# Kernel optimization log

Measured on AMD Instinct MI355X. Metric: run time of the kernel, lower is better.

## Reference

```python
import jax, jax.numpy as jnp
from jax import lax
import numpy as np

L = 4          # n_layers
H = 1024       # hidden_units
IN = 128       # input feature dim
OUT = 128      # out_size
B = 64         # batch
T = 512        # seq_len


def setup_inputs() -> dict:
    key = jax.random.key(0)
    ks = jax.random.split(key, 10)
    def glorot(k, shape):
        fan_in, fan_out = shape[-2], shape[-1]
        lim = np.sqrt(6.0 / (fan_in + fan_out)).astype(np.float32)
        return jax.random.uniform(k, shape, jnp.float32, -lim, lim)
    return {
        "x": jax.random.normal(ks[0], (B, T, IN), jnp.float32),
        "Wi": glorot(ks[1], (IN, H)),          # i_proj kernel
        "bi": jnp.zeros((H,), jnp.float32),     # i_proj bias
        "Wh": glorot(ks[2], (L, 2 * H, H)),     # per-layer Dense(Wh) kernel on concat([x,h])
        "bh_dense": jnp.zeros((L, H), jnp.float32),  # Dense(Wh) bias
        "bh": jnp.zeros((L, H), jnp.float32),        # extra bh weight
        "Wy": glorot(ks[3], (L, H, H)),         # per-layer Dense(Wy) kernel
        "by_dense": jnp.zeros((L, H), jnp.float32),  # Dense(Wy) bias
        "by": jnp.zeros((L, H), jnp.float32),        # extra by weight
        "Wo": glorot(ks[4], (H, OUT)),          # o_proj kernel
        "bo_dense": jnp.zeros((OUT,), jnp.float32),  # o_proj bias
        "o_bias": jnp.zeros((OUT,), jnp.float32),    # extra o_bias weight
    }


def reference(x, Wi, bi, Wh, bh_dense, bh, Wy, by_dense, by, Wo, bo_dense, o_bias):
    # decode() path, dropout as identity (deterministic reference).
    x_proj = x @ Wi + bi                      # [B, T, H]
    xs = jnp.transpose(x_proj, (1, 0, 2))     # time-major [T, B, H]
    h0 = jnp.zeros((L, B, H), x.dtype)

    def step(h_prev, xt):                     # h_prev [L,B,H], xt [B,H]
        inp = xt
        h_new = []
        for m in range(L):
            xc = jnp.concatenate([inp, h_prev[m]], axis=1)          # [B, 2H]
            h = jax.nn.relu(xc @ Wh[m] + bh_dense[m] + bh[m])       # [B, H]
            y = h @ Wy[m] + by_dense[m] + by[m]                     # [B, H]
            out = y + inp          # RNNLayer residual
            out = out + inp        # RNNNetwork residual (applied twice, faithful)
            h_new.append(h)
            inp = out
        return jnp.stack(h_new, axis=0), inp

    _, dec_states = lax.scan(step, h0, xs)    # dec_states [T, B, H]
    dec_states = jnp.transpose(dec_states, (1, 0, 2))  # [B, T, H]
    return dec_states @ Wo + bo_dense + o_bias         # [B, T, OUT]
```

## Files before the change

### kernel.cpp

```cpp
#include <hip/hip_runtime.h>
#include <cstdint>
#include <cstddef>

namespace {
constexpr int HD  = 1024;
constexpr int LD  = 4;
constexpr int BD  = 64;
constexpr int TD  = 512;
constexpr int IND = 128;
constexpr int OD  = 128;
constexpr int NSLOT = 5;
constexpr int LBH = LD * BD * HD;
constexpr int BH  = BD * HD;
constexpr int UNITS = 2816;
constexpr size_t HH = (size_t)HD * HD;
}

typedef unsigned short ushort_t;
typedef __attribute__((ext_vector_type(8))) short short8x;
typedef __attribute__((ext_vector_type(4))) float f32x4;

__device__ __forceinline__ ushort_t f2bf(float f) {
  unsigned u = __builtin_bit_cast(unsigned, f);
  u += 0x7FFFu + ((u >> 16) & 1u);
  return (ushort_t)(u >> 16);
}
__device__ __forceinline__ float bf2f(ushort_t h) {
  return __builtin_bit_cast(float, (unsigned)h << 16);
}
__device__ __forceinline__ void split3(float f, ushort_t& h1, ushort_t& h2, ushort_t& h3) {
  h1 = f2bf(f); float r = f - bf2f(h1);
  h2 = f2bf(r); r -= bf2f(h2);
  h3 = f2bf(r);
}

__device__ __forceinline__ void gemm_tile(
    const float* __restrict__ A, int lda, const float* __restrict__ Bm, int ldb,
    float* __restrict__ C, int ldc, int K, int row0, int col0,
    float alpha, const float* __restrict__ addvec)
{
  __shared__ float a_lds[64][65];
  __shared__ __align__(16) float b_lds[64][132];
  const int tid = threadIdx.x;
  const int rg = tid >> 4, cg = tid & 15;

  float acc[4][8];
  #pragma unroll
  for (int i = 0; i < 4; ++i)
    #pragma unroll
    for (int j = 0; j < 8; ++j) acc[i][j] = 0.f;

  for (int k0 = 0; k0 < K; k0 += 64) {
    #pragma unroll
    for (int i = 0; i < 4; ++i) {
      const int q = tid + i * 256;
      const int r = q >> 4;
      const int k4 = (q & 15) << 2;
      const float4 v = *(const float4*)(A + (size_t)(row0 + r) * lda + k0 + k4);
      a_lds[r][k4 + 0] = v.x; a_lds[r][k4 + 1] = v.y;
      a_lds[r][k4 + 2] = v.z; a_lds[r][k4 + 3] = v.w;
    }
    #pragma unroll
    for (int i = 0; i < 8; ++i) {
      const int q = tid + i * 256;
      const int k = q >> 5;
      const int c4 = (q & 31) << 2;
      *(float4*)&b_lds[k][c4] = *(const float4*)(Bm + (size_t)(k0 + k) * ldb + col0 + c4);
    }
    __syncthreads();
    #pragma unroll 4
    for (int k = 0; k < 64; ++k) {
      float wv[8], av[4];
      *(float4*)&wv[0] = *(const float4*)&b_lds[k][cg * 8];
      *(float4*)&wv[4] = *(const float4*)&b_lds[k][cg * 8 + 4];
      #pragma unroll
      for (int i = 0; i < 4; ++i) av[i] = a_lds[rg * 4 + i][k];
      #pragma unroll
      for (int i = 0; i < 4; ++i)
        #pragma unroll
        for (int j = 0; j < 8; ++j)
          acc[i][j] = fmaf(av[i], wv[j], acc[i][j]);
    }
    __syncthreads();
  }

  #pragma unroll
  for (int i = 0; i < 4; ++i) {
    const int r = row0 + rg * 4 + i;
    #pragma unroll
    for (int j = 0; j < 8; ++j) {
      const int c = col0 + cg * 8 + j;
      float v = alpha * acc[i][j];
      if (addvec) v += addvec[c];
      C[(size_t)r * ldc + c] = v;
    }
  }
}

__global__ __launch_bounds__(256) void prep1_k(
    const float* __restrict__ Wy, const float* __restrict__ Wh,
    const float* __restrict__ Wi, const float* __restrict__ Wo,
    float* __restrict__ G, float* __restrict__ WiA,
    float* __restrict__ P, float* __restrict__ WiWo)
{
  static const int pj[6] = {0, 0, 1, 0, 1, 2};
  static const int pm[6] = {1, 2, 2, 3, 3, 3};
  const int bid = blockIdx.x;
  const float *A, *Bm; float* C; int lda, ldb, ldc, row0, col0;
  if (bid < 768) {
    const int p = bid >> 7, rr = bid & 127;
    A = Wy + (size_t)pj[p] * HH; lda = HD;
    Bm = Wh + (size_t)pm[p] * 2 * HH; ldb = HD;
    C = G + (size_t)p * HH; ldc = HD;
    row0 = (rr >> 3) * 64; col0 = (rr & 7) * 128;
  } else if (bid < 832) {
    const int r = bid - 768, m = r >> 4;
    A = Wi; lda = HD;
    Bm = Wh + (size_t)m * 2 * HH; ldb = HD;
    C = WiA + (size_t)m * IND * HD; ldc = HD;
    row0 = ((r >> 3) & 1) * 64; col0 = (r & 7) * 128;
  } else if (bid < 896) {
    const int r = bid - 832, j = r >> 4;
    A = Wy + (size_t)j * HH; lda = HD;
    Bm = Wo; ldb = OD;
    C = P + (size_t)j * HD * OD; ldc = OD;
    row0 = (r & 15) * 64; col0 = 0;
  } else {
    const int r = bid - 896;
    A = Wi; lda = HD; Bm = Wo; ldb = OD; C = WiWo; ldc = OD;
    row0 = r * 64; col0 = 0;
  }
  gemm_tile(A, lda, Bm, ldb, C, ldc, HD, row0, col0, 1.f, nullptr);
}

__global__ __launch_bounds__(256) void prep2_k(
    const float* __restrict__ x, const float* __restrict__ WiWo,
    const float* __restrict__ const_o, float* __restrict__ out)
{
  gemm_tile(x, IND, WiWo, OD, out, OD, IND, blockIdx.x * 64, 0, 16.f, const_o);
}

__global__ __launch_bounds__(256) void consts_k(
    const float* __restrict__ Wh, const float* __restrict__ bh_dense, const float* __restrict__ bh,
    const float* __restrict__ by_dense, const float* __restrict__ by, const float* __restrict__ bi,
    const float* __restrict__ Wo, const float* __restrict__ bo_dense, const float* __restrict__ o_bias,
    float* __restrict__ cvec, float* __restrict__ const_o)
{
  __shared__ float e_lds[HD];
  const int tid = threadIdx.x;
  if (blockIdx.x < 16) {
    const int m = blockIdx.x >> 2;
    const int hcol = ((blockIdx.x & 3) << 8) + tid;
    for (int k = tid; k < HD; k += 256) {
      float e = (float)(1 << m) * bi[k];
      for (int j = 0; j < m; ++j)
        e += (float)(1 << (m - 1 - j)) * (by_dense[j * HD + k] + by[j * HD + k]);
      e_lds[k] = e;
    }
    __syncthreads();
    float acc = bh_dense[m * HD + hcol] + bh[m * HD + hcol];
    for (int k = 0; k < HD; ++k)
      acc = fmaf(e_lds[k], Wh[(size_t)m * 2 * HH + (size_t)k * HD + hcol], acc);
    cvec[m * HD + hcol] = acc;
  } else {
    if (tid < OD) {
      float acc = bo_dense[tid] + o_bias[tid];
      for (int k = 0; k < HD; ++k) {
        float e = 16.f * bi[k];
        e += 8.f * (by_dense[0 * HD + k] + by[0 * HD + k]);
        e += 4.f * (by_dense[1 * HD + k] + by[1 * HD + k]);
        e += 2.f * (by_dense[2 * HD + k] + by[2 * HD + k]);
        e += 1.f * (by_dense[3 * HD + k] + by[3 * HD + k]);
        acc = fmaf(e, Wo[(size_t)k * OD + tid], acc);
      }
      const_o[tid] = acc;
    }
  }
}

__global__ __launch_bounds__(256) void prep3_k(
    const float* __restrict__ G, const float* __restrict__ Wh,
    const float* __restrict__ WiA, const float* __restrict__ P,
    ushort_t* __restrict__ wTh, ushort_t* __restrict__ wTx, ushort_t* __restrict__ wTp)
{
  __shared__ ushort_t tl[3][64][66];
  const int tid = threadIdx.x, bid = blockIdx.x;
  const float* src; ushort_t* dstb; int ld, dstK, k0, n0; size_t PS;
  if (bid < 2560) {
    const int mat = bid >> 8, rr = bid & 255;
    k0 = (rr >> 4) * 64; n0 = (rr & 15) * 64;
    src = (mat < 6) ? (G + (size_t)mat * HH) : (Wh + (size_t)(mat - 6) * 2 * HH + HH);
    ld = 1024; dstb = wTh + (size_t)mat * 3 * HH; PS = HH; dstK = 1024;
  } else if (bid < 2688) {
    const int r = bid - 2560, mat = r >> 5, rr = r & 31;
    k0 = (rr >> 4) * 64; n0 = (rr & 15) * 64;
    src = WiA + (size_t)mat * IND * HD; ld = 1024;
    dstb = wTx + (size_t)mat * 3 * 131072; PS = 131072; dstK = 128;
  } else {
    const int r = bid - 2688, mat = r >> 5, rr = r & 31;
    k0 = (rr >> 1) * 64; n0 = (rr & 1) * 64;
    src = P + (size_t)mat * HD * OD; ld = 128;
    dstb = wTp + (size_t)mat * 3 * 131072; PS = 131072; dstK = 1024;
  }
  #pragma unroll
  for (int i = 0; i < 4; ++i) {
    const int q = tid + i * 256, kr = q >> 4, n4 = (q & 15) * 4;
    const float4 vv = *(const float4*)(src + (size_t)(k0 + kr) * ld + n0 + n4);
    ushort_t h1, h2, h3;
    split3(vv.x, h1, h2, h3); tl[0][n4+0][kr]=h1; tl[1][n4+0][kr]=h2; tl[2][n4+0][kr]=h3;
    split3(vv.y, h1, h2, h3); tl[0][n4+1][kr]=h1; tl[1][n4+1][kr]=h2; tl[2][n4+1][kr]=h3;
    split3(vv.z, h1, h2, h3); tl[0][n4+2][kr]=h1; tl[1][n4+2][kr]=h2; tl[2][n4+2][kr]=h3;
    split3(vv.w, h1, h2, h3); tl[0][n4+3][kr]=h1; tl[1][n4+3][kr]=h2; tl[2][n4+3][kr]=h3;
  }
  __syncthreads();
  #pragma unroll
  for (int i = 0; i < 4; ++i) {
    const int q = tid + i * 256, nr = q >> 4, k4 = (q & 15) * 4;
    #pragma unroll
    for (int p = 0; p < 3; ++p) {
      const unsigned lo = (unsigned)tl[p][nr][k4]     | ((unsigned)tl[p][nr][k4+1] << 16);
      const unsigned hi = (unsigned)tl[p][nr][k4 + 2] | ((unsigned)tl[p][nr][k4+3] << 16);
      *(uint2*)(dstb + (size_t)p * PS + (size_t)(n0 + nr) * dstK + k0 + k4) = make_uint2(lo, hi);
    }
  }
}

__global__ __launch_bounds__(256, 3) void rnn_scan_k(
    const float* __restrict__ x,
    const ushort_t* __restrict__ wTh,
    const ushort_t* __restrict__ wTx,
    const ushort_t* __restrict__ wTp,
    const float* __restrict__ cvec,
    float* __restrict__ zring,
    float* __restrict__ outp,
    int* __restrict__ bar, int nblk)
{
  __shared__ __align__(16) ushort_t s_a[3 * 64 * 64];
  __shared__ __align__(16) ushort_t s_b[3 * 64 * 64];
  const int tid = threadIdx.x, bid = blockIdx.x;
  const int lane = tid & 63, wid = tid >> 6;
  const int qr = wid >> 1, qc = wid & 1;
  const int l15 = lane & 15, l4 = lane >> 4;
  const int arow0 = tid & 63, akq = tid >> 6;
  const int bcol = tid >> 2, bks = tid & 3;
  const int u0 = (UNITS * bid) / nblk;
  const int u1 = (UNITS * (bid + 1)) / nblk;
  const int gb[4] = {0, 0, 1, 3};

  const int ar0 = qr * 32 + l15, ar1 = ar0 + 16;
  const int bc0 = qc * 32 + l15, bc1 = bc0 + 16;
  const int oa0b = ar0 * 64, oa1b = ar1 * 64, ob0b = bc0 * 64, ob1b = bc1 * 64;
  const int as0 = ar0 & 7, as1 = ar1 & 7, bs0 = bc0 & 7, bs1 = bc1 & 7;

  int* root = bar + 1024;
  int* gen  = bar + 1056;

  for (int v = 0; v < TD + LD; ++v) {
    {
      float* zp = zring + (size_t)((v + 1) % NSLOT) * LBH;
      for (int i = bid * 256 + tid; i < LBH; i += nblk * 256)
        __hip_atomic_store(&zp[i], 0.f, __ATOMIC_RELAXED, __HIP_MEMORY_SCOPE_AGENT);
    }

    f32x4 c00 = {0.f,0.f,0.f,0.f}, c01 = c00, c10 = c00, c11 = c00;
    float* cur = nullptr;
    int cldd = 0;

    auto flush = [&]() {
      const int colb = qc * 32 + l15;
      const int rowb = qr * 32 + l4 * 4;
      #pragma unroll
      for (int r = 0; r < 4; ++r) {
        atomicAdd(cur + (size_t)(rowb + r) * cldd + colb,           c00[r]);
        atomicAdd(cur + (size_t)(rowb + r) * cldd + colb + 16,      c01[r]);
        atomicAdd(cur + (size_t)(rowb + 16 + r) * cldd + colb,      c10[r]);
        atomicAdd(cur + (size_t)(rowb + 16 + r) * cldd + colb + 16, c11[r]);
      }
      c00 = f32x4{0.f,0.f,0.f,0.f}; c01 = c00; c10 = c00; c11 = c00;
    };

    for (int u = u0; u < u1; ++u) {
      const float* Ab = nullptr; const float* cvp = nullptr;
      const ushort_t* Wt = nullptr;
      float* dst = nullptr;
      int Ars = 0, WK = 0, dstrs = 0; size_t WPS = 0;
      float scale = 1.f;

      if (u < 2688) {
        int m, rel;
        if (u < 288)       { m = 0; rel = u; }
        else if (u < 832)  { m = 1; rel = u - 288; }
        else if (u < 1632) { m = 2; rel = u - 832; }
        else               { m = 3; rel = u - 1632; }
        const int per = (m + 1) * 16 + 2;
        const int cb = rel / per, r2 = rel - cb * per;
        const int t = v - m;
        if (t >= 0 && t < TD) {
          if (r2 < (m + 1) * 16) {
            const int src = r2 >> 4, kc = r2 & 15;
            if (src < m) {
              const int j = src;
              Ab  = zring + (size_t)((t + j) % NSLOT) * LBH + (size_t)j * BH + kc * 64;
              cvp = cvec + j * HD + kc * 64;
              scale = (float)(1 << (m - 1 - j));
              Wt = wTh + (size_t)(gb[m] + j) * 3 * HH + (size_t)(cb * 64) * 1024 + kc * 64;
              Ars = HD; WPS = HH; WK = 1024;
              dst = zring + (size_t)(v % NSLOT) * LBH + (size_t)m * BH + cb * 64;
              dstrs = HD;
            } else if (t >= 1) {
              Ab  = zring + (size_t)((v - 1) % NSLOT) * LBH + (size_t)m * BH + kc * 64;
              cvp = cvec + m * HD + kc * 64;
              scale = 1.f;
              Wt = wTh + (size_t)(6 + m) * 3 * HH + (size_t)(cb * 64) * 1024 + kc * 64;
              Ars = HD; WPS = HH; WK = 1024;
              dst = zring + (size_t)(v % NSLOT) * LBH + (size_t)m * BH + cb * 64;
              dstrs = HD;
            }
          } else {
            const int xk = r2 - (m + 1) * 16;
            Ab = x + (size_t)t * IND + xk * 64;
            Ars = TD * IND; cvp = nullptr;
            scale = (float)(1 << m);
            Wt = wTx + (size_t)m * 3 * 131072 + (size_t)(cb * 64) * 128 + xk * 64;
            WPS = 131072; WK = 128;
            dst = zring + (size_t)(v % NSLOT) * LBH + (size_t)m * BH + cb * 64;
            dstrs = HD;
          }
        }
      } else {
        const int r = u - 2688, j = r >> 5, rr = r & 31, ct = rr >> 4, kc = rr & 15;
        const int tp = v - 1 - j;
        if (tp >= 0 && tp < TD) {
          Ab  = zring + (size_t)((v - 1) % NSLOT) * LBH + (size_t)j * BH + kc * 64;
          Ars = HD;
          cvp = cvec + j * HD + kc * 64;
          scale = (float)(1 << (3 - j));
          Wt = wTp + (size_t)j * 3 * 131072 + (size_t)(ct * 64) * 1024 + kc * 64;
          WPS = 131072; WK = 1024;
          dst = outp + (size_t)tp * OD + ct * 64;
          dstrs = TD * OD;
        }
      }
      if (!Ab || !Wt) continue;

      if (dst != cur) {
        if (cur) flush();
        cur = dst; cldd = dstrs;
      }

      {
        const int swz = arow0 & 7;
        #pragma unroll
        for (int j = 0; j < 4; ++j) {
          const int k4 = akq * 16 + j * 4;
          float4 vv = *(const float4*)(Ab + (size_t)arow0 * Ars + k4);
          if (cvp) {
            const float4 c4 = *(const float4*)(cvp + k4);
            vv.x = fmaxf(vv.x + c4.x, 0.f);
            vv.y = fmaxf(vv.y + c4.y, 0.f);
            vv.z = fmaxf(vv.z + c4.z, 0.f);
            vv.w = fmaxf(vv.w + c4.w, 0.f);
          }
          vv.x *= scale; vv.y *= scale; vv.z *= scale; vv.w *= scale;
          ushort_t x1,x2,x3, y1,y2,y3, z1,z2,z3, w1,w2,w3;
          split3(vv.x, x1,x2,x3); split3(vv.y, y1,y2,y3);
          split3(vv.z, z1,z2,z3); split3(vv.w, w1,w2,w3);
          const int slot = k4 >> 3, half = (k4 >> 2) & 1;
          const int off = arow0 * 64 + 8 * (slot ^ swz) + half * 4;
          *(uint2*)(s_a + off)        = make_uint2((unsigned)x1 | ((unsigned)y1 << 16),
                                                   (unsigned)z1 | ((unsigned)w1 << 16));
          *(uint2*)(s_a + 4096 + off) = make_uint2((unsigned)x2 | ((unsigned)y2 << 16),
                                                   (unsigned)z2 | ((unsigned)w2 << 16));
          *(uint2*)(s_a + 8192 + off) = make_uint2((unsigned)x3 | ((unsigned)y3 << 16),
                                                   (unsigned)z3 | ((unsigned)w3 << 16));
        }
      }
      {
        const int csw = bcol & 7;
        #pragma unroll
        for (int p = 0; p < 3; ++p) {
          const ushort_t* wp = Wt + (size_t)p * WPS + (size_t)bcol * WK;
          const uint4 f0 = *(const uint4*)(wp + bks * 8);
          const uint4 f1 = *(const uint4*)(wp + 32 + bks * 8);
          ushort_t* bb = s_b + p * 4096 + bcol * 64;
          *(uint4*)(bb + 8 * (bks ^ csw))       = f0;
          *(uint4*)(bb + 8 * ((bks + 4) ^ csw)) = f1;
        }
      }
      __syncthreads();

      #pragma unroll
      for (int s = 0; s < 2; ++s) {
        const int sl = s * 4 + l4;
        const int oa0 = oa0b + 8 * (sl ^ as0);
        const int oa1 = oa1b + 8 * (sl ^ as1);
        const int ob0 = ob0b + 8 * (sl ^ bs0);
        const int ob1 = ob1b + 8 * (sl ^ bs1);
        const short8x A01 = *(const short8x*)(s_a + oa0);
        const short8x A02 = *(const short8x*)(s_a + 4096 + oa0);
        const short8x A03 = *(const short8x*)(s_a + 8192 + oa0);
        const short8x A11 = *(const short8x*)(s_a + oa1);
        const short8x A12 = *(const short8x*)(s_a + 4096 + oa1);
        const short8x A13 = *(const short8x*)(s_a + 8192 + oa1);
        const short8x B01 = *(const short8x*)(s_b + ob0);
        const short8x B02 = *(const short8x*)(s_b + 4096 + ob0);
        const short8x B03 = *(const short8x*)(s_b + 8192 + ob0);
        const short8x B11 = *(const short8x*)(s_b + ob1);
        const short8x B12 = *(const short8x*)(s_b + 4096 + ob1);
        const short8x B13 = *(const short8x*)(s_b + 8192 + ob1);
        c00 = __builtin_amdgcn_mfma_f32_16x16x32_bf16(A01, B01, c00, 0, 0, 0);
        c00 = __builtin_amdgcn_mfma_f32_16x16x32_bf16(A01, B02, c00, 0, 0, 0);
        c00 = __builtin_amdgcn_mfma_f32_16x16x32_bf16(A02, B01, c00, 0, 0, 0);
        c00 = __builtin_amdgcn_mfma_f32_16x16x32_bf16(A01, B03, c00, 0, 0, 0);
        c00 = __builtin_amdgcn_mfma_f32_16x16x32_bf16(A02, B02, c00, 0, 0, 0);
        c00 = __builtin_amdgcn_mfma_f32_16x16x32_bf16(A03, B01, c00, 0, 0, 0);
        c01 = __builtin_amdgcn_mfma_f32_16x16x32_bf16(A01, B11, c01, 0, 0, 0);
        c01 = __builtin_amdgcn_mfma_f32_16x16x32_bf16(A01, B12, c01, 0, 0, 0);
        c01 = __builtin_amdgcn_mfma_f32_16x16x32_bf16(A02, B11, c01, 0, 0, 0);
        c01 = __builtin_amdgcn_mfma_f32_16x16x32_bf16(A01, B13, c01, 0, 0, 0);
        c01 = __builtin_amdgcn_mfma_f32_16x16x32_bf16(A02, B12, c01, 0, 0, 0);
        c01 = __builtin_amdgcn_mfma_f32_16x16x32_bf16(A03, B11, c01, 0, 0, 0);
        c10 = __builtin_amdgcn_mfma_f32_16x16x32_bf16(A11, B01, c10, 0, 0, 0);
        c10 = __builtin_amdgcn_mfma_f32_16x16x32_bf16(A11, B02, c10, 0, 0, 0);
        c10 = __builtin_amdgcn_mfma_f32_16x16x32_bf16(A12, B01, c10, 0, 0, 0);
        c10 = __builtin_amdgcn_mfma_f32_16x16x32_bf16(A11, B03, c10, 0, 0, 0);
        c10 = __builtin_amdgcn_mfma_f32_16x16x32_bf16(A12, B02, c10, 0, 0, 0);
        c10 = __builtin_amdgcn_mfma_f32_16x16x32_bf16(A13, B01, c10, 0, 0, 0);
        c11 = __builtin_amdgcn_mfma_f32_16x16x32_bf16(A11, B11, c11, 0, 0, 0);
        c11 = __builtin_amdgcn_mfma_f32_16x16x32_bf16(A11, B12, c11, 0, 0, 0);
        c11 = __builtin_amdgcn_mfma_f32_16x16x32_bf16(A12, B11, c11, 0, 0, 0);
        c11 = __builtin_amdgcn_mfma_f32_16x16x32_bf16(A11, B13, c11, 0, 0, 0);
        c11 = __builtin_amdgcn_mfma_f32_16x16x32_bf16(A12, B12, c11, 0, 0, 0);
        c11 = __builtin_amdgcn_mfma_f32_16x16x32_bf16(A13, B11, c11, 0, 0, 0);
      }
      __syncthreads();
    }

    if (cur) flush();

    __syncthreads();
    if (tid == 0) {
      int* leaf = bar + (bid & 31) * 32;
      const int lc = nblk >> 5;
      const int p = __hip_atomic_fetch_add(leaf, 1, __ATOMIC_ACQ_REL, __HIP_MEMORY_SCOPE_AGENT);
      if (p == (v + 1) * lc - 1) {
        const int q = __hip_atomic_fetch_add(root, 1, __ATOMIC_ACQ_REL, __HIP_MEMORY_SCOPE_AGENT);
        if (q == (v + 1) * 32 - 1) {
          __hip_atomic_store(gen, v + 1, __ATOMIC_RELEASE, __HIP_MEMORY_SCOPE_AGENT);
        } else {
          while (__hip_atomic_load(gen, __ATOMIC_RELAXED, __HIP_MEMORY_SCOPE_AGENT) < v + 1)
            __builtin_amdgcn_s_sleep(2);
          __builtin_amdgcn_fence(__ATOMIC_ACQUIRE, "agent");
        }
      } else {
        while (__hip_atomic_load(gen, __ATOMIC_RELAXED, __HIP_MEMORY_SCOPE_AGENT) < v + 1)
          __builtin_amdgcn_s_sleep(2);
        __builtin_amdgcn_fence(__ATOMIC_ACQUIRE, "agent");
      }
    }
    __syncthreads();
  }
}

extern "C" void kernel_launch(void* const* d_in, const int* in_sizes, int n_in,
                              void* d_out, int out_size, void* d_ws, size_t ws_size,
                              hipStream_t stream)
{
  (void)in_sizes; (void)n_in; (void)out_size; (void)ws_size;

  const float* x        = (const float*)d_in[0];
  const float* Wi       = (const float*)d_in[1];
  const float* bi       = (const float*)d_in[2];
  const float* Wh       = (const float*)d_in[3];
  const float* bh_dense = (const float*)d_in[4];
  const float* bh       = (const float*)d_in[5];
  const float* Wy       = (const float*)d_in[6];
  const float* by_dense = (const float*)d_in[7];
  const float* by       = (const float*)d_in[8];
  const float* Wo       = (const float*)d_in[9];
  const float* bo_dense = (const float*)d_in[10];
  const float* o_bias   = (const float*)d_in[11];
  float* out = (float*)d_out;
  float* ws  = (float*)d_ws;

  size_t off = 0;
  float* G       = ws + off; off += (size_t)6 * HH;
  float* WiA     = ws + off; off += (size_t)4 * IND * HD;
  float* P       = ws + off; off += (size_t)4 * HD * OD;
  float* WiWo    = ws + off; off += (size_t)IND * OD;
  float* cvec    = ws + off; off += (size_t)4 * HD;
  float* const_o = ws + off; off += OD;
  off = (off + 63) & ~(size_t)63;
  float* zring   = ws + off; off += (size_t)NSLOT * LBH;
  int*   bar     = (int*)(ws + off); off += 4096;
  ushort_t* wTh  = (ushort_t*)(ws + off); off += (size_t)10 * 3 * HH / 2;
  ushort_t* wTx  = (ushort_t*)(ws + off); off += (size_t)4 * 3 * 131072 / 2;
  ushort_t* wTp  = (ushort_t*)(ws + off); off += (size_t)4 * 3 * 131072 / 2;

  int occ = 2;
  if (hipOccupancyMaxActiveBlocksPerMultiprocessor(&occ, rnn_scan_k, 256, 0) != hipSuccess)
    occ = 2;
  if (occ < 1) occ = 1;
  if (occ > 3) occ = 3;
  const int nblk = 256 * occ;

  hipMemsetAsync(zring, 0, (size_t)NSLOT * LBH * sizeof(float) + 16384, stream);

  consts_k<<<17, 256, 0, stream>>>(Wh, bh_dense, bh, by_dense, by, bi,
                                   Wo, bo_dense, o_bias, cvec, const_o);
  prep1_k<<<898, 256, 0, stream>>>(Wy, Wh, Wi, Wo, G, WiA, P, WiWo);
  prep2_k<<<512, 256, 0, stream>>>(x, WiWo, const_o, out);
  prep3_k<<<2816, 256, 0, stream>>>(G, Wh, WiA, P, wTh, wTx, wTp);
  rnn_scan_k<<<nblk, 256, 0, stream>>>(x, wTh, wTx, wTp, cvec, zring, out, bar, nblk);
}
```

Before: 20.16 ms.

## Pack per-unit weight tiles into pre-swizzled blobs and double-buffer async LDS loads

The prep pass now stores each work unit's split-bf16 weight tile as one contiguous, pre-swizzled blob. The scan kernel streams the next unit's blob straight into LDS with global_load_lds, double-buffered, so the weight fetch overlaps the current unit's MFMA work and skips the register round trip. The activation staging is also rewritten to wider vector stores, and split3 truncates the first two parts instead of rounding them. Doubling the B buffer raises LDS use and caps occupancy at 2 blocks per CU instead of 3, which could reduce latency hiding.

```diff
diff --git a/kernel.cpp b/kernel.cpp
--- a/kernel.cpp
+++ b/kernel.cpp
@@ -14,24 +14,58 @@
 constexpr int BH  = BD * HD;
 constexpr int UNITS = 2816;
 constexpr size_t HH = (size_t)HD * HD;
+constexpr int BLOB_US = 12288;
 }
 
 typedef unsigned short ushort_t;
 typedef __attribute__((ext_vector_type(8))) short short8x;
 typedef __attribute__((ext_vector_type(4))) float f32x4;
 
-__device__ __forceinline__ ushort_t f2bf(float f) {
+__device__ __forceinline__ ushort_t f2bf_rne(float f) {
   unsigned u = __builtin_bit_cast(unsigned, f);
   u += 0x7FFFu + ((u >> 16) & 1u);
   return (ushort_t)(u >> 16);
 }
-__device__ __forceinline__ float bf2f(ushort_t h) {
-  return __builtin_bit_cast(float, (unsigned)h << 16);
-}
 __device__ __forceinline__ void split3(float f, ushort_t& h1, ushort_t& h2, ushort_t& h3) {
-  h1 = f2bf(f); float r = f - bf2f(h1);
-  h2 = f2bf(r); r -= bf2f(h2);
-  h3 = f2bf(r);
+  const unsigned u = __builtin_bit_cast(unsigned, f);
+  h1 = (ushort_t)(u >> 16);
+  const float r = f - __builtin_bit_cast(float, u & 0xFFFF0000u);
+  const unsigned u2 = __builtin_bit_cast(unsigned, r);
+  h2 = (ushort_t)(u2 >> 16);
+  const float r2 = r - __builtin_bit_cast(float, u2 & 0xFFFF0000u);
+  h3 = f2bf_rne(r2);
+}
+
+struct WSrc { const float* base; int ld; int k0; int n0; };
+__device__ __forceinline__ WSrc unit_wsrc(
+    int u, const float* G, const float* Wh, const float* WiA, const float* P)
+{
+  const int gb[4] = {0, 0, 1, 3};
+  WSrc w;
+  if (u < 2688) {
+    int m, rel;
+    if (u < 288)       { m = 0; rel = u; }
+    else if (u < 832)  { m = 1; rel = u - 288; }
+    else if (u < 1632) { m = 2; rel = u - 832; }
+    else               { m = 3; rel = u - 1632; }
+    const int per = (m + 1) * 16 + 2;
+    const int cb = rel / per, r2 = rel - cb * per;
+    if (r2 < (m + 1) * 16) {
+      const int src = r2 >> 4, kc = r2 & 15;
+      if (src < m) w.base = G + (size_t)(gb[m] + src) * HH;
+      else         w.base = Wh + (size_t)m * 2 * HH + HH;
+      w.ld = HD; w.k0 = kc * 64; w.n0 = cb * 64;
+    } else {
+      const int xk = r2 - (m + 1) * 16;
+      w.base = WiA + (size_t)m * IND * HD;
+      w.ld = HD; w.k0 = xk * 64; w.n0 = cb * 64;
+    }
+  } else {
+    const int r = u - 2688, j = r >> 5, rr = r & 31, ct = rr >> 4, kc = rr & 15;
+    w.base = P + (size_t)j * HD * OD;
+    w.ld = OD; w.k0 = kc * 64; w.n0 = ct * 64;
+  }
+  return w;
 }
 
 __device__ __forceinline__ void gemm_tile(
@@ -181,31 +215,18 @@
 __global__ __launch_bounds__(256) void prep3_k(
     const float* __restrict__ G, const float* __restrict__ Wh,
     const float* __restrict__ WiA, const float* __restrict__ P,
-    ushort_t* __restrict__ wTh, ushort_t* __restrict__ wTx, ushort_t* __restrict__ wTp)
+    ushort_t* __restrict__ blobs)
 {
   __shared__ ushort_t tl[3][64][66];
-  const int tid = threadIdx.x, bid = blockIdx.x;
-  const float* src; ushort_t* dstb; int ld, dstK, k0, n0; size_t PS;
-  if (bid < 2560) {
-    const int mat = bid >> 8, rr = bid & 255;
-    k0 = (rr >> 4) * 64; n0 = (rr & 15) * 64;
-    src = (mat < 6) ? (G + (size_t)mat * HH) : (Wh + (size_t)(mat - 6) * 2 * HH + HH);
-    ld = 1024; dstb = wTh + (size_t)mat * 3 * HH; PS = HH; dstK = 1024;
-  } else if (bid < 2688) {
-    const int r = bid - 2560, mat = r >> 5, rr = r & 31;
-    k0 = (rr >> 4) * 64; n0 = (rr & 15) * 64;
-    src = WiA + (size_t)mat * IND * HD; ld = 1024;
-    dstb = wTx + (size_t)mat * 3 * 131072; PS = 131072; dstK = 128;
-  } else {
-    const int r = bid - 2688, mat = r >> 5, rr = r & 31;
-    k0 = (rr >> 1) * 64; n0 = (rr & 1) * 64;
-    src = P + (size_t)mat * HD * OD; ld = 128;
-    dstb = wTp + (size_t)mat * 3 * 131072; PS = 131072; dstK = 1024;
-  }
+  const int tid = threadIdx.x;
+  const int u = blockIdx.x;
+  const WSrc w = unit_wsrc(u, G, Wh, WiA, P);
+
   #pragma unroll
   for (int i = 0; i < 4; ++i) {
-    const int q = tid + i * 256, kr = q >> 4, n4 = (q & 15) * 4;
-    const float4 vv = *(const float4*)(src + (size_t)(k0 + kr) * ld + n0 + n4);
+    const int q = tid + i * 256;
+    const int kr = q >> 4, n4 = (q & 15) * 4;
+    const float4 vv = *(const float4*)(w.base + (size_t)(w.k0 + kr) * w.ld + w.n0 + n4);
     ushort_t h1, h2, h3;
     split3(vv.x, h1, h2, h3); tl[0][n4+0][kr]=h1; tl[1][n4+0][kr]=h2; tl[2][n4+0][kr]=h3;
     split3(vv.y, h1, h2, h3); tl[0][n4+1][kr]=h1; tl[1][n4+1][kr]=h2; tl[2][n4+1][kr]=h3;
@@ -213,36 +234,49 @@
     split3(vv.w, h1, h2, h3); tl[0][n4+3][kr]=h1; tl[1][n4+3][kr]=h2; tl[2][n4+3][kr]=h3;
   }
   __syncthreads();
+
+  ushort_t* ob = blobs + (size_t)u * BLOB_US;
   #pragma unroll
-  for (int i = 0; i < 4; ++i) {
-    const int q = tid + i * 256, nr = q >> 4, k4 = (q & 15) * 4;
+  for (int i = 0; i < 2; ++i) {
+    const int idx = tid + i * 256;
+    const int c = idx >> 3, s8 = idx & 7;
     #pragma unroll
     for (int p = 0; p < 3; ++p) {
-      const unsigned lo = (unsigned)tl[p][nr][k4]     | ((unsigned)tl[p][nr][k4+1] << 16);
-      const unsigned hi = (unsigned)tl[p][nr][k4 + 2] | ((unsigned)tl[p][nr][k4+3] << 16);
-      *(uint2*)(dstb + (size_t)p * PS + (size_t)(n0 + nr) * dstK + k0 + k4) = make_uint2(lo, hi);
-    }
-  }
-}
-
-__global__ __launch_bounds__(256, 3) void rnn_scan_k(
+      const ushort_t* t8 = &tl[p][c][s8 * 8];
+      const unsigned w0 = (unsigned)t8[0] | ((unsigned)t8[1] << 16);
+      const unsigned w1 = (unsigned)t8[2] | ((unsigned)t8[3] << 16);
+      const unsigned w2 = (unsigned)t8[4] | ((unsigned)t8[5] << 16);
+      const unsigned w3 = (unsigned)t8[6] | ((unsigned)t8[7] << 16);
+      *(uint4*)(ob + p * 4096 + c * 64 + 8 * (s8 ^ (c & 7))) = make_uint4(w0, w1, w2, w3);
+    }
+  }
+}
+
+__device__ __forceinline__ void issue_dma(const ushort_t* g, ushort_t* l, int wid, int lane) {
+  const char* gs = (const char*)g + wid * 6144 + lane * 16;
+  char* ls = (char*)l + wid * 6144;
+  #pragma unroll
+  for (int i = 0; i < 6; ++i)
+    __builtin_amdgcn_global_load_lds(
+        (const __attribute__((address_space(1))) void*)(gs + i * 1024),
+        (__attribute__((address_space(3))) void*)(ls + i * 1024), 16, 0, 0);
+}
+
+__global__ __launch_bounds__(256, 2) void rnn_scan_k(
     const float* __restrict__ x,
-    const ushort_t* __restrict__ wTh,
-    const ushort_t* __restrict__ wTx,
-    const ushort_t* __restrict__ wTp,
+    const ushort_t* __restrict__ blobs,
     const float* __restrict__ cvec,
     float* __restrict__ zring,
     float* __restrict__ outp,
     int* __restrict__ bar, int nblk)
 {
-  __shared__ __align__(16) ushort_t s_a[3 * 64 * 64];
-  __shared__ __align__(16) ushort_t s_b[3 * 64 * 64];
+  __shared__ __align__(16) ushort_t s_a[3 * 4096];
+  __shared__ __align__(16) ushort_t s_b[2 * 3 * 4096];
   const int tid = threadIdx.x, bid = blockIdx.x;
   const int lane = tid & 63, wid = tid >> 6;
   const int qr = wid >> 1, qc = wid & 1;
   const int l15 = lane & 15, l4 = lane >> 4;
-  const int arow0 = tid & 63, akq = tid >> 6;
-  const int bcol = tid >> 2, bks = tid & 3;
+  const int ar_r = tid >> 2, ar_kq = tid & 3;
   const int u0 = (UNITS * bid) / nblk;
   const int u1 = (UNITS * (bid + 1)) / nblk;
   const int gb[4] = {0, 0, 1, 3};
@@ -254,6 +288,9 @@
 
   int* root = bar + 1024;
   int* gen  = bar + 1056;
+
+  issue_dma(blobs + (size_t)u0 * BLOB_US, s_b, wid, lane);
+  int pbuf = 0;
 
   for (int v = 0; v < TD + LD; ++v) {
     {
@@ -281,9 +318,8 @@
 
     for (int u = u0; u < u1; ++u) {
       const float* Ab = nullptr; const float* cvp = nullptr;
-      const ushort_t* Wt = nullptr;
       float* dst = nullptr;
-      int Ars = 0, WK = 0, dstrs = 0; size_t WPS = 0;
+      int Ars = 0, dstrs = 0;
       float scale = 1.f;
 
       if (u < 2688) {
@@ -303,16 +339,14 @@
               Ab  = zring + (size_t)((t + j) % NSLOT) * LBH + (size_t)j * BH + kc * 64;
               cvp = cvec + j * HD + kc * 64;
               scale = (float)(1 << (m - 1 - j));
-              Wt = wTh + (size_t)(gb[m] + j) * 3 * HH + (size_t)(cb * 64) * 1024 + kc * 64;
-              Ars = HD; WPS = HH; WK = 1024;
+              Ars = HD;
               dst = zring + (size_t)(v % NSLOT) * LBH + (size_t)m * BH + cb * 64;
               dstrs = HD;
             } else if (t >= 1) {
               Ab  = zring + (size_t)((v - 1) % NSLOT) * LBH + (size_t)m * BH + kc * 64;
               cvp = cvec + m * HD + kc * 64;
               scale = 1.f;
-              Wt = wTh + (size_t)(6 + m) * 3 * HH + (size_t)(cb * 64) * 1024 + kc * 64;
-              Ars = HD; WPS = HH; WK = 1024;
+              Ars = HD;
               dst = zring + (size_t)(v % NSLOT) * LBH + (size_t)m * BH + cb * 64;
               dstrs = HD;
             }
@@ -321,8 +355,6 @@
             Ab = x + (size_t)t * IND + xk * 64;
             Ars = TD * IND; cvp = nullptr;
             scale = (float)(1 << m);
-            Wt = wTx + (size_t)m * 3 * 131072 + (size_t)(cb * 64) * 128 + xk * 64;
-            WPS = 131072; WK = 128;
             dst = zring + (size_t)(v % NSLOT) * LBH + (size_t)m * BH + cb * 64;
             dstrs = HD;
           }
@@ -335,105 +367,112 @@
           Ars = HD;
           cvp = cvec + j * HD + kc * 64;
           scale = (float)(1 << (3 - j));
-          Wt = wTp + (size_t)j * 3 * 131072 + (size_t)(ct * 64) * 1024 + kc * 64;
-          WPS = 131072; WK = 1024;
           dst = outp + (size_t)tp * OD + ct * 64;
           dstrs = TD * OD;
         }
       }
-      if (!Ab || !Wt) continue;
-
-      if (dst != cur) {
+      const bool active = (Ab != nullptr);
+
+      if (active && dst != cur) {
         if (cur) flush();
         cur = dst; cldd = dstrs;
       }
 
+      if (active) {
+        float vv[16];
+        const float* ap = Ab + (size_t)ar_r * (size_t)Ars + ar_kq * 16;
+        *(float4*)&vv[0]  = *(const float4*)(ap + 0);
+        *(float4*)&vv[4]  = *(const float4*)(ap + 4);
+        *(float4*)&vv[8]  = *(const float4*)(ap + 8);
+        *(float4*)&vv[12] = *(const float4*)(ap + 12);
+        if (cvp) {
+          const float* cp2 = cvp + ar_kq * 16;
+          #pragma unroll
+          for (int e = 0; e < 16; ++e) vv[e] = fmaxf(vv[e] + cp2[e], 0.f);
+        }
+        #pragma unroll
+        for (int e = 0; e < 16; ++e) vv[e] *= scale;
+        #pragma unroll
+        for (int i = 0; i < 2; ++i) {
+          unsigned p1[4], p2[4], p3[4];
+          #pragma unroll
+          for (int q2 = 0; q2 < 4; ++q2) {
+            ushort_t a1, a2, a3, b1, b2, b3;
+            split3(vv[i * 8 + q2 * 2],     a1, a2, a3);
+            split3(vv[i * 8 + q2 * 2 + 1], b1, b2, b3);
+            p1[q2] = (unsigned)a1 | ((unsigned)b1 << 16);
+            p2[q2] = (unsigned)a2 | ((unsigned)b2 << 16);
+            p3[q2] = (unsigned)a3 | ((unsigned)b3 << 16);
+          }
+          const int s8 = ar_kq * 2 + i;
+          const int off = ar_r * 64 + 8 * (s8 ^ (ar_r & 7));
+          *(uint4*)(s_a + off)        = make_uint4(p1[0], p1[1], p1[2], p1[3]);
+          *(uint4*)(s_a + 4096 + off) = make_uint4(p2[0], p2[1], p2[2], p2[3]);
+          *(uint4*)(s_a + 8192 + off) = make_uint4(p3[0], p3[1], p3[2], p3[3]);
+        }
+      }
+
+      asm volatile("" ::: "memory");
       {
-        const int swz = arow0 & 7;
+        const int nu = (u + 1 < u1) ? (u + 1) : u0;
+        issue_dma(blobs + (size_t)nu * BLOB_US, s_b + (pbuf ^ 1) * BLOB_US, wid, lane);
+      }
+      asm volatile("s_waitcnt lgkmcnt(0)" ::: "memory");
+      __builtin_amdgcn_s_barrier();
+      __builtin_amdgcn_sched_barrier(0);
+
+      if (active) {
+        const ushort_t* sbb = s_b + pbuf * BLOB_US;
         #pragma unroll
-        for (int j = 0; j < 4; ++j) {
-          const int k4 = akq * 16 + j * 4;
-          float4 vv = *(const float4*)(Ab + (size_t)arow0 * Ars + k4);
-          if (cvp) {
-            const float4 c4 = *(const float4*)(cvp + k4);
-            vv.x = fmaxf(vv.x + c4.x, 0.f);
-            vv.y = fmaxf(vv.y + c4.y, 0.f);
-            vv.z = fmaxf(vv.z + c4.z, 0.f);
-            vv.w = fmaxf(vv.w + c4.w, 0.f);
-          }
-          vv.x *= scale; vv.y *= scale; vv.z *= scale; vv.w *= scale;
-          ushort_t x1,x2,x3, y1,y2,y3, z1,z2,z3, w1,w2,w3;
-          split3(vv.x, x1,x2,x3); split3(vv.y, y1,y2,y3);
-          split3(vv.z, z1,z2,z3); split3(vv.w, w1,w2,w3);
-          const int slot = k4 >> 3, half = (k4 >> 2) & 1;
-          const int off = arow0 * 64 + 8 * (slot ^ swz) + half * 4;
-          *(uint2*)(s_a + off)        = make_uint2((unsigned)x1 | ((unsigned)y1 << 16),
-                                                   (unsigned)z1 | ((unsigned)w1 << 16));
-          *(uint2*)(s_a + 4096 + off) = make_uint2((unsigned)x2 | ((unsigned)y2 << 16),
-                                                   (unsigned)z2 | ((unsigned)w2 << 16));
-          *(uint2*)(s_a + 8192 + off) = make_uint2((unsigned)x3 | ((unsigned)y3 << 16),
-                                                   (unsigned)z3 | ((unsigned)w3 << 16));
+        for (int s = 0; s < 2; ++s) {
+          const int sl = s * 4 + l4;
+          const int oa0 = oa0b + 8 * (sl ^ as0);
+          const int oa1 = oa1b + 8 * (sl ^ as1);
+          const int ob0 = ob0b + 8 * (sl ^ bs0);
+          const int ob1 = ob1b + 8 * (sl ^ bs1);
+          const short8x A01 = *(const short8x*)(s_a + oa0);
+          const short8x A02 = *(const short8x*)(s_a + 4096 + oa0);
+          const short8x A03 = *(const short8x*)(s_a + 8192 + oa0);
+          const short8x A11 = *(const short8x*)(s_a + oa1);
+          const short8x A12 = *(const short8x*)(s_a + 4096 + oa1);
+          const short8x A13 = *(const short8x*)(s_a + 8192 + oa1);
+          const short8x B01 = *(const short8x*)(sbb + ob0);
+          const short8x B02 = *(const short8x*)(sbb + 4096 + ob0);
+          const short8x B03 = *(const short8x*)(sbb + 8192 + ob0);
+          const short8x B11 = *(const short8x*)(sbb + ob1);
+          const short8x B12 = *(const short8x*)(sbb + 4096 + ob1);
+          const short8x B13 = *(const short8x*)(sbb + 8192 + ob1);
+          c00 = __builtin_amdgcn_mfma_f32_16x16x32_bf16(A01, B01, c00, 0, 0, 0);
+          c00 = __builtin_amdgcn_mfma_f32_16x16x32_bf16(A01, B02, c00, 0, 0, 0);
+          c00 = __builtin_amdgcn_mfma_f32_16x16x32_bf16(A02, B01, c00, 0, 0, 0);
+          c00 = __builtin_amdgcn_mfma_f32_16x16x32_bf16(A01, B03, c00, 0, 0, 0);
+          c00 = __builtin_amdgcn_mfma_f32_16x16x32_bf16(A02, B02, c00, 0, 0, 0);
+          c00 = __builtin_amdgcn_mfma_f32_16x16x32_bf16(A03, B01, c00, 0, 0, 0);
+          c01 = __builtin_amdgcn_mfma_f32_16x16x32_bf16(A01, B11, c01, 0, 0, 0);
+          c01 = __builtin_amdgcn_mfma_f32_16x16x32_bf16(A01, B12, c01, 0, 0, 0);
+          c01 = __builtin_amdgcn_mfma_f32_16x16x32_bf16(A02, B11, c01, 0, 0, 0);
+          c01 = __builtin_amdgcn_mfma_f32_16x16x32_bf16(A01, B13, c01, 0, 0, 0);
+          c01 = __builtin_amdgcn_mfma_f32_16x16x32_bf16(A02, B12, c01, 0, 0, 0);
+          c01 = __builtin_amdgcn_mfma_f32_16x16x32_bf16(A03, B11, c01, 0, 0, 0);
+          c10 = __builtin_amdgcn_mfma_f32_16x16x32_bf16(A11, B01, c10, 0, 0, 0);
+          c10 = __builtin_amdgcn_mfma_f32_16x16x32_bf16(A11, B02, c10, 0, 0, 0);
+          c10 = __builtin_amdgcn_mfma_f32_16x16x32_bf16(A12, B01, c10, 0, 0, 0);
+          c10 = __builtin_amdgcn_mfma_f32_16x16x32_bf16(A11, B03, c10, 0, 0, 0);
+          c10 = __builtin_amdgcn_mfma_f32_16x16x32_bf16(A12, B02, c10, 0, 0, 0);
+          c10 = __builtin_amdgcn_mfma_f32_16x16x32_bf16(A13, B01, c10, 0, 0, 0);
+          c11 = __builtin_amdgcn_mfma_f32_16x16x32_bf16(A11, B11, c11, 0, 0, 0);
+          c11 = __builtin_amdgcn_mfma_f32_16x16x32_bf16(A11, B12, c11, 0, 0, 0);
+          c11 = __builtin_amdgcn_mfma_f32_16x16x32_bf16(A12, B11, c11, 0, 0, 0);
+          c11 = __builtin_amdgcn_mfma_f32_16x16x32_bf16(A11, B13, c11, 0, 0, 0);
+          c11 = __builtin_amdgcn_mfma_f32_16x16x32_bf16(A12, B12, c11, 0, 0, 0);
+          c11 = __builtin_amdgcn_mfma_f32_16x16x32_bf16(A13, B11, c11, 0, 0, 0);
         }
       }
-      {
-        const int csw = bcol & 7;
-        #pragma unroll
-        for (int p = 0; p < 3; ++p) {
-          const ushort_t* wp = Wt + (size_t)p * WPS + (size_t)bcol * WK;
-          const uint4 f0 = *(const uint4*)(wp + bks * 8);
-          const uint4 f1 = *(const uint4*)(wp + 32 + bks * 8);
-          ushort_t* bb = s_b + p * 4096 + bcol * 64;
-          *(uint4*)(bb + 8 * (bks ^ csw))       = f0;
-          *(uint4*)(bb + 8 * ((bks + 4) ^ csw)) = f1;
-        }
-      }
-      __syncthreads();
-
-      #pragma unroll
-      for (int s = 0; s < 2; ++s) {
-        const int sl = s * 4 + l4;
-        const int oa0 = oa0b + 8 * (sl ^ as0);
-        const int oa1 = oa1b + 8 * (sl ^ as1);
-        const int ob0 = ob0b + 8 * (sl ^ bs0);
-        const int ob1 = ob1b + 8 * (sl ^ bs1);
-        const short8x A01 = *(const short8x*)(s_a + oa0);
-        const short8x A02 = *(const short8x*)(s_a + 4096 + oa0);
-        const short8x A03 = *(const short8x*)(s_a + 8192 + oa0);
-        const short8x A11 = *(const short8x*)(s_a + oa1);
-        const short8x A12 = *(const short8x*)(s_a + 4096 + oa1);
-        const short8x A13 = *(const short8x*)(s_a + 8192 + oa1);
-        const short8x B01 = *(const short8x*)(s_b + ob0);
-        const short8x B02 = *(const short8x*)(s_b + 4096 + ob0);
-        const short8x B03 = *(const short8x*)(s_b + 8192 + ob0);
-        const short8x B11 = *(const short8x*)(s_b + ob1);
-        const short8x B12 = *(const short8x*)(s_b + 4096 + ob1);
-        const short8x B13 = *(const short8x*)(s_b + 8192 + ob1);
-        c00 = __builtin_amdgcn_mfma_f32_16x16x32_bf16(A01, B01, c00, 0, 0, 0);
-        c00 = __builtin_amdgcn_mfma_f32_16x16x32_bf16(A01, B02, c00, 0, 0, 0);
-        c00 = __builtin_amdgcn_mfma_f32_16x16x32_bf16(A02, B01, c00, 0, 0, 0);
-        c00 = __builtin_amdgcn_mfma_f32_16x16x32_bf16(A01, B03, c00, 0, 0, 0);
-        c00 = __builtin_amdgcn_mfma_f32_16x16x32_bf16(A02, B02, c00, 0, 0, 0);
-        c00 = __builtin_amdgcn_mfma_f32_16x16x32_bf16(A03, B01, c00, 0, 0, 0);
-        c01 = __builtin_amdgcn_mfma_f32_16x16x32_bf16(A01, B11, c01, 0, 0, 0);
-        c01 = __builtin_amdgcn_mfma_f32_16x16x32_bf16(A01, B12, c01, 0, 0, 0);
-        c01 = __builtin_amdgcn_mfma_f32_16x16x32_bf16(A02, B11, c01, 0, 0, 0);
-        c01 = __builtin_amdgcn_mfma_f32_16x16x32_bf16(A01, B13, c01, 0, 0, 0);
-        c01 = __builtin_amdgcn_mfma_f32_16x16x32_bf16(A02, B12, c01, 0, 0, 0);
-        c01 = __builtin_amdgcn_mfma_f32_16x16x32_bf16(A03, B11, c01, 0, 0, 0);
-        c10 = __builtin_amdgcn_mfma_f32_16x16x32_bf16(A11, B01, c10, 0, 0, 0);
-        c10 = __builtin_amdgcn_mfma_f32_16x16x32_bf16(A11, B02, c10, 0, 0, 0);
-        c10 = __builtin_amdgcn_mfma_f32_16x16x32_bf16(A12, B01, c10, 0, 0, 0);
-        c10 = __builtin_amdgcn_mfma_f32_16x16x32_bf16(A11, B03, c10, 0, 0, 0);
-        c10 = __builtin_amdgcn_mfma_f32_16x16x32_bf16(A12, B02, c10, 0, 0, 0);
-        c10 = __builtin_amdgcn_mfma_f32_16x16x32_bf16(A13, B01, c10, 0, 0, 0);
-        c11 = __builtin_amdgcn_mfma_f32_16x16x32_bf16(A11, B11, c11, 0, 0, 0);
-        c11 = __builtin_amdgcn_mfma_f32_16x16x32_bf16(A11, B12, c11, 0, 0, 0);
-        c11 = __builtin_amdgcn_mfma_f32_16x16x32_bf16(A12, B11, c11, 0, 0, 0);
-        c11 = __builtin_amdgcn_mfma_f32_16x16x32_bf16(A11, B13, c11, 0, 0, 0);
-        c11 = __builtin_amdgcn_mfma_f32_16x16x32_bf16(A12, B12, c11, 0, 0, 0);
-        c11 = __builtin_amdgcn_mfma_f32_16x16x32_bf16(A13, B11, c11, 0, 0, 0);
-      }
-      __syncthreads();
+
+      asm volatile("s_waitcnt lgkmcnt(0)" ::: "memory");
+      __builtin_amdgcn_s_barrier();
+      __builtin_amdgcn_sched_barrier(0);
+      pbuf ^= 1;
     }
 
     if (cur) flush();
@@ -493,15 +532,14 @@
   off = (off + 63) & ~(size_t)63;
   float* zring   = ws + off; off += (size_t)NSLOT * LBH;
   int*   bar     = (int*)(ws + off); off += 4096;
-  ushort_t* wTh  = (ushort_t*)(ws + off); off += (size_t)10 * 3 * HH / 2;
-  ushort_t* wTx  = (ushort_t*)(ws + off); off += (size_t)4 * 3 * 131072 / 2;
-  ushort_t* wTp  = (ushort_t*)(ws + off); off += (size_t)4 * 3 * 131072 / 2;
+  off = (off + 15) & ~(size_t)15;
+  ushort_t* blobs = (ushort_t*)(ws + off);
 
   int occ = 2;
   if (hipOccupancyMaxActiveBlocksPerMultiprocessor(&occ, rnn_scan_k, 256, 0) != hipSuccess)
     occ = 2;
   if (occ < 1) occ = 1;
-  if (occ > 3) occ = 3;
+  if (occ > 2) occ = 2;
   const int nblk = 256 * occ;
 
   hipMemsetAsync(zring, 0, (size_t)NSLOT * LBH * sizeof(float) + 16384, stream);
@@ -510,6 +548,6 @@
                                    Wo, bo_dense, o_bias, cvec, const_o);
   prep1_k<<<898, 256, 0, stream>>>(Wy, Wh, Wi, Wo, G, WiA, P, WiWo);
   prep2_k<<<512, 256, 0, stream>>>(x, WiWo, const_o, out);
-  prep3_k<<<2816, 256, 0, stream>>>(G, Wh, WiA, P, wTh, wTx, wTp);
-  rnn_scan_k<<<nblk, 256, 0, stream>>>(x, wTh, wTx, wTp, cvec, zring, out, bar, nblk);
-}
+  prep3_k<<<UNITS, 256, 0, stream>>>(G, Wh, WiA, P, blobs);
+  rnn_scan_k<<<nblk, 256, 0, stream>>>(x, blobs, cvec, zring, out, bar, nblk);
+}
```

Result: faster. 18.04 ms (-10.5%).
